# Kernel optimization log

Measured on AMD Instinct MI355X. Metric: run time of the kernel, lower is better.

The kernel has to match this reference:

```python
import jax, jax.numpy as jnp
import numpy as np

B, S, D, H = 4, 2048, 1024, 16
HD = D // H  # head dim = 64


def setup_inputs() -> dict:
    key = jax.random.key(0)
    ks = jax.random.split(key, 11)
    scale = 1.0 / np.sqrt(D)
    return {
        "q": jax.random.normal(ks[0], (B, S, D), jnp.float32),
        "k": jax.random.normal(ks[1], (B, S, D), jnp.float32),
        "v": jax.random.normal(ks[2], (B, S, D), jnp.float32),
        "w_q": jax.random.normal(ks[3], (D, D), jnp.float32) * scale,
        "b_q": jax.random.normal(ks[4], (D,), jnp.float32) * scale,
        "w_k": jax.random.normal(ks[5], (D, D), jnp.float32) * scale,
        "b_k": jax.random.normal(ks[6], (D,), jnp.float32) * scale,
        "w_v": jax.random.normal(ks[7], (D, D), jnp.float32) * scale,
        "b_v": jax.random.normal(ks[8], (D,), jnp.float32) * scale,
        "w_o": jax.random.normal(ks[9], (D, D), jnp.float32) * scale,
        "b_o": jax.random.normal(ks[10], (D,), jnp.float32) * scale,
    }


def _split_heads(x):
    # [B,S,D] -> [B,H,S,HD]
    return x.reshape(B, S, H, HD).transpose(0, 2, 1, 3)


def reference(q, k, v, w_q, b_q, w_k, b_k, w_v, b_v, w_o, b_o):
    qh = _split_heads(q @ w_q + b_q)
    kh = _split_heads(k @ w_k + b_k)
    vh = _split_heads(v @ w_v + b_v)
    # full score matrix [B,H,S,S], as in the naive torch code
    score = jnp.einsum("bhqd,bhkd->bhqk", qh, kh) / jnp.sqrt(jnp.float32(HD))
    attn = jax.nn.softmax(score, axis=-1)
    out = jnp.einsum("bhqk,bhkd->bhqd", attn, vh)
    out = out.transpose(0, 2, 1, 3).reshape(B, S, D)
    return out @ w_o + b_o
```

## Files before the change

### kernel.cpp

```cpp
#include <hip/hip_runtime.h>
#include <hip/hip_bf16.h>

#define BB 4
#define SS 2048
#define DD 1024
#define HH 16
#define HDD 64
#define MM (BB*SS)

using bf16x8 = __attribute__((ext_vector_type(8))) short;
using f32x4  = __attribute__((ext_vector_type(4))) float;
using f32x16 = __attribute__((ext_vector_type(16))) float;

static __device__ __forceinline__ ushort f2bf(float f) {
    __hip_bfloat16 h = __float2bfloat16(f);
    return *reinterpret_cast<ushort*>(&h);
}

static __device__ __forceinline__ void gload_lds16(const ushort* g, ushort* l) {
    __builtin_amdgcn_global_load_lds(
        (const __attribute__((address_space(1))) unsigned int*)g,
        (__attribute__((address_space(3))) unsigned int*)l, 16, 0, 0);
}

static __device__ __forceinline__ unsigned cvtpk(float lo, float hi) {
    unsigned r;
    asm("v_cvt_pk_bf16_f32 %0, %1, %2" : "=v"(r) : "v"(lo), "v"(hi));
    return r;
}

static __device__ __forceinline__ float exp2_raw(float x) {
    float r;
    asm("v_exp_f32 %0, %1" : "=v"(r) : "v"(x));
    return r;
}

static __device__ __forceinline__ void halfswap(unsigned& a, unsigned& b, int hi) {
#if __has_builtin(__builtin_amdgcn_permlane32_swap)
    typedef int v2i __attribute__((ext_vector_type(2)));
    v2i r = __builtin_amdgcn_permlane32_swap((int)a, (int)b, false, false);
    a = (unsigned)r.x; b = (unsigned)r.y;
#else
    unsigned xa = (unsigned)__shfl_xor((int)a, 32);
    unsigned xb = (unsigned)__shfl_xor((int)b, 32);
    unsigned na = hi ? xb : a;
    unsigned nb = hi ? b : xa;
    a = na; b = nb;
#endif
}

#define PIPE_BAR(N) do {                                          \
    asm volatile("s_waitcnt vmcnt(" #N ")" ::: "memory");         \
    __builtin_amdgcn_sched_barrier(0);                            \
    __builtin_amdgcn_s_barrier();                                 \
    __builtin_amdgcn_sched_barrier(0);                            \
} while (0)

__global__ __launch_bounds__(256) void cast3_bf16_k(
    const float* __restrict__ q, const float* __restrict__ k,
    const float* __restrict__ v, ushort* __restrict__ qo,
    ushort* __restrict__ ko, ushort* __restrict__ vo)
{
    const float* in; ushort* out;
    switch (blockIdx.y) {
        case 0:  in = q; out = qo; break;
        case 1:  in = k; out = ko; break;
        default: in = v; out = vo; break;
    }
    const size_t i = ((size_t)blockIdx.x * 256 + threadIdx.x) * 8;
    float4 a = *(const float4*)(in + i);
    float4 b = *(const float4*)(in + i + 4);
    short r[8];
    r[0] = (short)f2bf(a.x); r[1] = (short)f2bf(a.y);
    r[2] = (short)f2bf(a.z); r[3] = (short)f2bf(a.w);
    r[4] = (short)f2bf(b.x); r[5] = (short)f2bf(b.y);
    r[6] = (short)f2bf(b.z); r[7] = (short)f2bf(b.w);
    *(bf16x8*)(out + i) = *(const bf16x8*)r;
}

__global__ __launch_bounds__(256) void wtrans_k(
    const float* __restrict__ w0, const float* __restrict__ w1,
    const float* __restrict__ w2, const float* __restrict__ w3,
    ushort* __restrict__ o0, ushort* __restrict__ o1,
    ushort* __restrict__ o2, ushort* __restrict__ o3)
{
    __shared__ float tile[32][33];
    const float* W; ushort* O;
    switch (blockIdx.z) {
        case 0:  W = w0; O = o0; break;
        case 1:  W = w1; O = o1; break;
        case 2:  W = w2; O = o2; break;
        default: W = w3; O = o3; break;
    }
    const int tx = threadIdx.x & 31, ty = threadIdx.x >> 5;
    const int n0 = blockIdx.x * 32, k0 = blockIdx.y * 32;
    #pragma unroll
    for (int i = 0; i < 4; i++)
        tile[ty * 4 + i][tx] = W[(size_t)(k0 + ty * 4 + i) * DD + n0 + tx];
    __syncthreads();
    #pragma unroll
    for (int i = 0; i < 4; i++)
        O[(size_t)(n0 + ty * 4 + i) * DD + k0 + tx] = f2bf(tile[tx][ty * 4 + i]);
}

template<int MODE>
__global__ __launch_bounds__(256) void gemm_mfma_k(
    const ushort* __restrict__ A, const ushort* __restrict__ WT,
    const float* __restrict__ bias, void* __restrict__ Cout)
{
    __shared__ ushort As[128 * 32];
    __shared__ ushort Bs[128 * 32];

    const int t  = threadIdx.x;
    const int w  = t >> 6;
    const int l  = t & 63;
    const int lr = l & 15;
    const int lg = l >> 4;
    const int wr = w >> 1, wc = w & 1;

    int bid = blockIdx.x;
    bid = (bid & 7) * 64 + (bid >> 3);
    const int mt = bid >> 3, nt = bid & 7;
    const int m0 = mt * 128, n0 = nt * 128;

    const int srow = l >> 2;
    const int scol = (l & 3) * 8;

    f32x4 acc[4][4];
    #pragma unroll
    for (int mi = 0; mi < 4; mi++)
        #pragma unroll
        for (int ni = 0; ni < 4; ni++)
            acc[mi][ni] = (f32x4){0.f, 0.f, 0.f, 0.f};

    const ushort* Ab = A  + (size_t)m0 * DD;
    const ushort* Bb = WT + (size_t)n0 * DD;

    for (int k0 = 0; k0 < DD; k0 += 32) {
        __syncthreads();
        #pragma unroll
        for (int j = 0; j < 2; j++) {
            const int rbase = (w * 2 + j) * 16;
            gload_lds16(Ab + (size_t)(rbase + srow) * DD + k0 + scol, &As[rbase * 32]);
            gload_lds16(Bb + (size_t)(rbase + srow) * DD + k0 + scol, &Bs[rbase * 32]);
        }
        __syncthreads();

        bf16x8 af[4], bfr[4];
        #pragma unroll
        for (int mi = 0; mi < 4; mi++)
            af[mi] = *(const bf16x8*)&As[(wr * 64 + mi * 16 + lr) * 32 + lg * 8];
        #pragma unroll
        for (int ni = 0; ni < 4; ni++)
            bfr[ni] = *(const bf16x8*)&Bs[(wc * 64 + ni * 16 + lr) * 32 + lg * 8];
        #pragma unroll
        for (int mi = 0; mi < 4; mi++)
            #pragma unroll
            for (int ni = 0; ni < 4; ni++)
                acc[mi][ni] = __builtin_amdgcn_mfma_f32_16x16x32_bf16(
                    af[mi], bfr[ni], acc[mi][ni], 0, 0, 0);
    }

    #pragma unroll
    for (int mi = 0; mi < 4; mi++) {
        #pragma unroll
        for (int ni = 0; ni < 4; ni++) {
            const int c  = n0 + wc * 64 + ni * 16 + lr;
            const float bc = bias[c];
            const int r0 = m0 + wr * 64 + mi * 16 + lg * 4;
            if (MODE == 0) {
                float* Co = (float*)Cout;
                #pragma unroll
                for (int rg = 0; rg < 4; rg++)
                    Co[(size_t)(r0 + rg) * DD + c] = acc[mi][ni][rg] + bc;
            } else if (MODE == 3) {
                const int bi = r0 >> 11, si = r0 & 2047;
                const int hi = c >> 6,  hd = c & 63;
                ushort pk[4];
                #pragma unroll
                for (int rg = 0; rg < 4; rg++)
                    pk[rg] = f2bf(acc[mi][ni][rg] + bc);
                ushort* O = (ushort*)Cout;
                *(uint2*)&O[(((size_t)(bi * HH + hi) * HDD) + hd) * SS + si] =
                    *(const uint2*)pk;
            } else {
                const float sc = (MODE == 2) ? 0.180336880111f : 1.0f;
                ushort* O = (ushort*)Cout;
                #pragma unroll
                for (int rg = 0; rg < 4; rg++) {
                    const int r = r0 + rg;
                    const int bi = r >> 11, si = r & 2047;
                    const int hi = c >> 6,  hd = c & 63;
                    O[(((size_t)(bi * HH + hi) * SS) + si) * HDD + hd] =
                        f2bf((acc[mi][ni][rg] + bc) * sc);
                }
            }
        }
    }
}

__global__ __launch_bounds__(256) void flash_attn_mfma(
    const ushort* __restrict__ qh, const ushort* __restrict__ kh,
    const ushort* __restrict__ vt, ushort* __restrict__ ctx)
{
    __shared__ ushort smem[24576];

    const int t  = threadIdx.x;
    const int w  = t >> 6;
    const int l  = t & 63;
    const int hi = l >> 5;
    const int lq = l & 31;

    const int wg = (blockIdx.x & 7) * 128 + (blockIdx.x >> 3);
    const int bi = wg >> 8;
    const int h  = (wg >> 4) & 15;
    const int q0 = (wg & 15) * 128;

    const size_t base  = (size_t)(bi * HH + h) * SS * HDD;
    const size_t basev = (size_t)(bi * HH + h) * HDD * SS;

    bf16x8 qf[4];
    {
        const ushort* qp = qh + base + (size_t)(q0 + w * 32 + lq) * HDD;
        #pragma unroll
        for (int ds = 0; ds < 4; ds++)
            qf[ds] = *(const bf16x8*)(qp + ds * 16 + hi * 8);
    }

    f32x16 o0 = {}, o1 = {};
    float l_loc = 0.f;

    const int rsub = l >> 3;
    const int csw  = ((l & 7) ^ rsub) * 8;
    auto stageK = [&](int buf, int kv) {
        #pragma unroll
        for (int j = 0; j < 2; j++) {
            const int rb = 16 * w + 8 * j;
            gload_lds16(kh + base + (size_t)(kv + rb + rsub) * HDD + csw,
                        &smem[buf * 4096 + rb * 64]);
        }
    };
    auto stageV = [&](int buf, int kv) {
        #pragma unroll
        for (int j = 0; j < 2; j++) {
            const int rb = 16 * w + 8 * j;
            gload_lds16(vt + basev + (size_t)(rb + rsub) * SS + kv + csw,
                        &smem[12288 + buf * 4096 + rb * 64]);
        }
    };

    auto qk = [&](int kbuf, f32x16& s0, f32x16& s1) {
        const ushort* KB = &smem[kbuf * 4096];
        s0 = (f32x16){};
        s1 = (f32x16){};
        __builtin_amdgcn_s_setprio(1);
        #pragma unroll
        for (int ds = 0; ds < 4; ds++) {
            const int slot = ((ds * 2 + hi) ^ (l & 7)) * 8;
            bf16x8 ka0 = *(const bf16x8*)&KB[lq * 64 + slot];
            bf16x8 ka1 = *(const bf16x8*)&KB[(32 + lq) * 64 + slot];
            s0 = __builtin_amdgcn_mfma_f32_32x32x16_bf16(ka0, qf[ds], s0, 0, 0, 0);
            s1 = __builtin_amdgcn_mfma_f32_32x32x16_bf16(ka1, qf[ds], s1, 0, 0, 0);
        }
        __builtin_amdgcn_s_setprio(0);
    };

    auto finish = [&](f32x16& s0, f32x16& s1, bf16x8* pa) {
        float t0 = 0.f, t1 = 0.f, t2 = 0.f, t3 = 0.f;
        #pragma unroll
        for (int r = 0; r < 16; r += 4) {
            s0[r + 0] = exp2_raw(s0[r + 0]); t0 += s0[r + 0];
            s0[r + 1] = exp2_raw(s0[r + 1]); t1 += s0[r + 1];
            s0[r + 2] = exp2_raw(s0[r + 2]); t2 += s0[r + 2];
            s0[r + 3] = exp2_raw(s0[r + 3]); t3 += s0[r + 3];
        }
        #pragma unroll
        for (int r = 0; r < 16; r += 4) {
            s1[r + 0] = exp2_raw(s1[r + 0]); t0 += s1[r + 0];
            s1[r + 1] = exp2_raw(s1[r + 1]); t1 += s1[r + 1];
            s1[r + 2] = exp2_raw(s1[r + 2]); t2 += s1[r + 2];
            s1[r + 3] = exp2_raw(s1[r + 3]); t3 += s1[r + 3];
        }
        l_loc += (t0 + t1) + (t2 + t3);
        #pragma unroll
        for (int sblk = 0; sblk < 4; sblk++) {
            const int ob = (sblk & 1) * 8;
            float e0, e1, e2, e3, e4, e5, e6, e7;
            if (sblk < 2) {
                e0 = s0[ob + 0]; e1 = s0[ob + 1]; e2 = s0[ob + 2]; e3 = s0[ob + 3];
                e4 = s0[ob + 4]; e5 = s0[ob + 5]; e6 = s0[ob + 6]; e7 = s0[ob + 7];
            } else {
                e0 = s1[ob + 0]; e1 = s1[ob + 1]; e2 = s1[ob + 2]; e3 = s1[ob + 3];
                e4 = s1[ob + 4]; e5 = s1[ob + 5]; e6 = s1[ob + 6]; e7 = s1[ob + 7];
            }
            unsigned a = cvtpk(e0, e1);
            unsigned b = cvtpk(e4, e5);
            halfswap(a, b, hi);
            unsigned c = cvtpk(e2, e3);
            unsigned d = cvtpk(e6, e7);
            halfswap(c, d, hi);
            union { unsigned u[4]; bf16x8 v; } fr;
            fr.u[0] = a; fr.u[1] = c; fr.u[2] = b; fr.u[3] = d;
            pa[sblk] = fr.v;
        }
    };

    auto pv = [&](int vbuf, const bf16x8* pa) {
        const ushort* VB = &smem[12288 + vbuf * 4096];
        __builtin_amdgcn_s_setprio(1);
        #pragma unroll
        for (int ks = 0; ks < 4; ks++) {
            const int slot = ((ks * 2 + hi) ^ (l & 7)) * 8;
            bf16x8 vb0 = *(const bf16x8*)&VB[lq * 64 + slot];
            bf16x8 vb1 = *(const bf16x8*)&VB[(32 + lq) * 64 + slot];
            o0 = __builtin_amdgcn_mfma_f32_32x32x16_bf16(pa[ks], vb0, o0, 0, 0, 0);
            o1 = __builtin_amdgcn_mfma_f32_32x32x16_bf16(pa[ks], vb1, o1, 0, 0, 0);
        }
        __builtin_amdgcn_s_setprio(0);
    };

    f32x16 sA0, sA1, sB0, sB1;
    bf16x8 pa[4];
    stageK(0, 0); stageK(1, 64); stageV(0, 0);
    PIPE_BAR(4);
    qk(0, sA0, sA1);

    int ka = 1, kb = 2, kc = 0;
    int va = 0, vb = 1, vc = 2;

    for (int tt = 0; tt < 30; tt += 2) {
        stageK(kb, (tt + 2) * 64);
        PIPE_BAR(2);
        stageV(vb, (tt + 1) * 64);
        qk(ka, sB0, sB1);
        finish(sA0, sA1, pa);
        pv(va, pa);
        { int k2 = ka; ka = kb; kb = kc; kc = k2;
          int v2 = va; va = vb; vb = vc; vc = v2; }

        stageK(kb, (tt + 3) * 64);
        PIPE_BAR(2);
        stageV(vb, (tt + 2) * 64);
        qk(ka, sA0, sA1);
        finish(sB0, sB1, pa);
        pv(va, pa);
        { int k2 = ka; ka = kb; kb = kc; kc = k2;
          int v2 = va; va = vb; vb = vc; vc = v2; }
    }

    PIPE_BAR(0);
    stageV(vb, 31 * 64);
    qk(ka, sB0, sB1);
    finish(sA0, sA1, pa);
    pv(va, pa);
    PIPE_BAR(0);
    finish(sB0, sB1, pa);
    pv(vb, pa);

    const float l_sum = l_loc + __shfl_xor(l_loc, 32);
    const float invl  = 1.0f / l_sum;
    #pragma unroll
    for (int r = 0; r < 16; r++) {
        const int qq = (r & 3) + 8 * (r >> 2) + 4 * hi;
        const float iv = __shfl(invl, qq);
        const int row = q0 + w * 32 + qq;
        ushort* op = ctx + (size_t)(bi * SS + row) * DD + h * HDD;
        op[lq]      = f2bf(o0[r] * iv);
        op[32 + lq] = f2bf(o1[r] * iv);
    }
}

extern "C" void kernel_launch(void* const* d_in, const int* in_sizes, int n_in,
                              void* d_out, int out_size, void* d_ws, size_t ws_size,
                              hipStream_t stream) {
    const float* q   = (const float*)d_in[0];
    const float* k   = (const float*)d_in[1];
    const float* v   = (const float*)d_in[2];
    const float* w_q = (const float*)d_in[3];
    const float* b_q = (const float*)d_in[4];
    const float* w_k = (const float*)d_in[5];
    const float* b_k = (const float*)d_in[6];
    const float* w_v = (const float*)d_in[7];
    const float* b_v = (const float*)d_in[8];
    const float* w_o = (const float*)d_in[9];
    const float* b_o = (const float*)d_in[10];
    float* out = (float*)d_out;

    const size_t SZ = (size_t)BB * SS * DD;
    const size_t WZ = (size_t)DD * DD;
    ushort* ws2  = (ushort*)d_ws;
    ushort* qh   = ws2;
    ushort* kh   = ws2 + SZ;
    ushort* vt   = ws2 + 2 * SZ;
    ushort* ctxb = ws2 + 3 * SZ;
    ushort* qbf  = ws2 + 4 * SZ;
    ushort* kbf  = ws2 + 5 * SZ;
    ushort* vbf  = ws2 + 6 * SZ;
    ushort* wqT  = ws2 + 7 * SZ;
    ushort* wkT  = wqT + WZ;
    ushort* wvT  = wkT + WZ;
    ushort* woT  = wvT + WZ;

    const int castBlocks = (int)(SZ / (256 * 8));
    cast3_bf16_k<<<dim3(castBlocks, 3), 256, 0, stream>>>(q, k, v, qbf, kbf, vbf);
    wtrans_k<<<dim3(32, 32, 4), 256, 0, stream>>>(w_q, w_k, w_v, w_o,
                                                  wqT, wkT, wvT, woT);

    const int gblocks = (MM / 128) * (DD / 128);
    gemm_mfma_k<2><<<gblocks, 256, 0, stream>>>(qbf, wqT, b_q, qh);
    gemm_mfma_k<1><<<gblocks, 256, 0, stream>>>(kbf, wkT, b_k, kh);
    gemm_mfma_k<3><<<gblocks, 256, 0, stream>>>(vbf, wvT, b_v, vt);

    flash_attn_mfma<<<dim3(1024), 256, 0, stream>>>(qh, kh, vt, ctxb);

    gemm_mfma_k<0><<<gblocks, 256, 0, stream>>>(ctxb, woT, b_o, out);
}
```

Baseline: 220.7 us.

## Double query rows per wave in flash attention and simplify to double-buffered pipeline

Each wave now handles 64 query rows (two 32-row groups) instead of 32, so each K/V tile loaded into LDS is reused across twice as many queries and the grid halves to 512 blocks. The triple-buffered K / software-pipelined QK-softmax-PV schedule is replaced with a simpler double-buffered loop that waits on every tile. LDS shrinks and launch bounds request two blocks per CU. This cuts LDS and global traffic per FLOP but raises register pressure and removes overlap of QK with the previous tile's softmax. With 512 blocks on a 256-CU device the occupancy may be thin.

```diff
diff --git a/kernel.cpp b/kernel.cpp
--- a/kernel.cpp
+++ b/kernel.cpp
@@ -199,11 +199,11 @@
     }
 }
 
-__global__ __launch_bounds__(256) void flash_attn_mfma(
+__global__ __launch_bounds__(256, 2) void flash_attn_mfma(
     const ushort* __restrict__ qh, const ushort* __restrict__ kh,
     const ushort* __restrict__ vt, ushort* __restrict__ ctx)
 {
-    __shared__ ushort smem[24576];
+    __shared__ ushort smem[16384];
 
     const int t  = threadIdx.x;
     const int w  = t >> 6;
@@ -211,24 +211,27 @@
     const int hi = l >> 5;
     const int lq = l & 31;
 
-    const int wg = (blockIdx.x & 7) * 128 + (blockIdx.x >> 3);
-    const int bi = wg >> 8;
-    const int h  = (wg >> 4) & 15;
-    const int q0 = (wg & 15) * 128;
+    const int wg = (blockIdx.x & 7) * 64 + (blockIdx.x >> 3);
+    const int bi = wg >> 7;
+    const int h  = (wg >> 3) & 15;
+    const int q0 = (wg & 7) * 256;
 
     const size_t base  = (size_t)(bi * HH + h) * SS * HDD;
     const size_t basev = (size_t)(bi * HH + h) * HDD * SS;
 
-    bf16x8 qf[4];
+    bf16x8 qf0[4], qf1[4];
     {
-        const ushort* qp = qh + base + (size_t)(q0 + w * 32 + lq) * HDD;
-        #pragma unroll
-        for (int ds = 0; ds < 4; ds++)
-            qf[ds] = *(const bf16x8*)(qp + ds * 16 + hi * 8);
-    }
-
-    f32x16 o0 = {}, o1 = {};
-    float l_loc = 0.f;
+        const ushort* qp0 = qh + base + (size_t)(q0 + w * 64 + lq) * HDD;
+        const ushort* qp1 = qp0 + 32 * HDD;
+        #pragma unroll
+        for (int ds = 0; ds < 4; ds++) {
+            qf0[ds] = *(const bf16x8*)(qp0 + ds * 16 + hi * 8);
+            qf1[ds] = *(const bf16x8*)(qp1 + ds * 16 + hi * 8);
+        }
+    }
+
+    f32x16 o00 = {}, o01 = {}, o10 = {}, o11 = {};
+    float l0 = 0.f, l1 = 0.f;
 
     const int rsub = l >> 3;
     const int csw  = ((l & 7) ^ rsub) * 8;
@@ -245,128 +248,108 @@
         for (int j = 0; j < 2; j++) {
             const int rb = 16 * w + 8 * j;
             gload_lds16(vt + basev + (size_t)(rb + rsub) * SS + kv + csw,
-                        &smem[12288 + buf * 4096 + rb * 64]);
+                        &smem[8192 + buf * 4096 + rb * 64]);
         }
     };
 
-    auto qk = [&](int kbuf, f32x16& s0, f32x16& s1) {
-        const ushort* KB = &smem[kbuf * 4096];
-        s0 = (f32x16){};
-        s1 = (f32x16){};
+    auto qk2 = [&](const ushort* KB, int kvh, f32x16& sg0, f32x16& sg1) {
+        sg0 = (f32x16){};
+        sg1 = (f32x16){};
         __builtin_amdgcn_s_setprio(1);
         #pragma unroll
         for (int ds = 0; ds < 4; ds++) {
             const int slot = ((ds * 2 + hi) ^ (l & 7)) * 8;
-            bf16x8 ka0 = *(const bf16x8*)&KB[lq * 64 + slot];
-            bf16x8 ka1 = *(const bf16x8*)&KB[(32 + lq) * 64 + slot];
-            s0 = __builtin_amdgcn_mfma_f32_32x32x16_bf16(ka0, qf[ds], s0, 0, 0, 0);
-            s1 = __builtin_amdgcn_mfma_f32_32x32x16_bf16(ka1, qf[ds], s1, 0, 0, 0);
+            bf16x8 ka = *(const bf16x8*)&KB[(kvh * 32 + lq) * 64 + slot];
+            sg0 = __builtin_amdgcn_mfma_f32_32x32x16_bf16(ka, qf0[ds], sg0, 0, 0, 0);
+            sg1 = __builtin_amdgcn_mfma_f32_32x32x16_bf16(ka, qf1[ds], sg1, 0, 0, 0);
         }
         __builtin_amdgcn_s_setprio(0);
     };
 
-    auto finish = [&](f32x16& s0, f32x16& s1, bf16x8* pa) {
+    auto finish16 = [&](f32x16& s, float& lacc, bf16x8* pa2) {
         float t0 = 0.f, t1 = 0.f, t2 = 0.f, t3 = 0.f;
         #pragma unroll
         for (int r = 0; r < 16; r += 4) {
-            s0[r + 0] = exp2_raw(s0[r + 0]); t0 += s0[r + 0];
-            s0[r + 1] = exp2_raw(s0[r + 1]); t1 += s0[r + 1];
-            s0[r + 2] = exp2_raw(s0[r + 2]); t2 += s0[r + 2];
-            s0[r + 3] = exp2_raw(s0[r + 3]); t3 += s0[r + 3];
-        }
-        #pragma unroll
-        for (int r = 0; r < 16; r += 4) {
-            s1[r + 0] = exp2_raw(s1[r + 0]); t0 += s1[r + 0];
-            s1[r + 1] = exp2_raw(s1[r + 1]); t1 += s1[r + 1];
-            s1[r + 2] = exp2_raw(s1[r + 2]); t2 += s1[r + 2];
-            s1[r + 3] = exp2_raw(s1[r + 3]); t3 += s1[r + 3];
-        }
-        l_loc += (t0 + t1) + (t2 + t3);
-        #pragma unroll
-        for (int sblk = 0; sblk < 4; sblk++) {
-            const int ob = (sblk & 1) * 8;
-            float e0, e1, e2, e3, e4, e5, e6, e7;
-            if (sblk < 2) {
-                e0 = s0[ob + 0]; e1 = s0[ob + 1]; e2 = s0[ob + 2]; e3 = s0[ob + 3];
-                e4 = s0[ob + 4]; e5 = s0[ob + 5]; e6 = s0[ob + 6]; e7 = s0[ob + 7];
-            } else {
-                e0 = s1[ob + 0]; e1 = s1[ob + 1]; e2 = s1[ob + 2]; e3 = s1[ob + 3];
-                e4 = s1[ob + 4]; e5 = s1[ob + 5]; e6 = s1[ob + 6]; e7 = s1[ob + 7];
-            }
-            unsigned a = cvtpk(e0, e1);
-            unsigned b = cvtpk(e4, e5);
+            s[r + 0] = exp2_raw(s[r + 0]); t0 += s[r + 0];
+            s[r + 1] = exp2_raw(s[r + 1]); t1 += s[r + 1];
+            s[r + 2] = exp2_raw(s[r + 2]); t2 += s[r + 2];
+            s[r + 3] = exp2_raw(s[r + 3]); t3 += s[r + 3];
+        }
+        lacc += (t0 + t1) + (t2 + t3);
+        #pragma unroll
+        for (int sblk = 0; sblk < 2; sblk++) {
+            const int ob = sblk * 8;
+            unsigned a = cvtpk(s[ob + 0], s[ob + 1]);
+            unsigned b = cvtpk(s[ob + 4], s[ob + 5]);
             halfswap(a, b, hi);
-            unsigned c = cvtpk(e2, e3);
-            unsigned d = cvtpk(e6, e7);
+            unsigned c = cvtpk(s[ob + 2], s[ob + 3]);
+            unsigned d = cvtpk(s[ob + 6], s[ob + 7]);
             halfswap(c, d, hi);
             union { unsigned u[4]; bf16x8 v; } fr;
             fr.u[0] = a; fr.u[1] = c; fr.u[2] = b; fr.u[3] = d;
-            pa[sblk] = fr.v;
+            pa2[sblk] = fr.v;
         }
     };
 
-    auto pv = [&](int vbuf, const bf16x8* pa) {
-        const ushort* VB = &smem[12288 + vbuf * 4096];
+    auto pvhalf = [&](const ushort* VB, int kvh,
+                      const bf16x8* pg0, const bf16x8* pg1) {
         __builtin_amdgcn_s_setprio(1);
         #pragma unroll
-        for (int ks = 0; ks < 4; ks++) {
+        for (int ksl = 0; ksl < 2; ksl++) {
+            const int ks = kvh * 2 + ksl;
             const int slot = ((ks * 2 + hi) ^ (l & 7)) * 8;
             bf16x8 vb0 = *(const bf16x8*)&VB[lq * 64 + slot];
             bf16x8 vb1 = *(const bf16x8*)&VB[(32 + lq) * 64 + slot];
-            o0 = __builtin_amdgcn_mfma_f32_32x32x16_bf16(pa[ks], vb0, o0, 0, 0, 0);
-            o1 = __builtin_amdgcn_mfma_f32_32x32x16_bf16(pa[ks], vb1, o1, 0, 0, 0);
+            o00 = __builtin_amdgcn_mfma_f32_32x32x16_bf16(pg0[ksl], vb0, o00, 0, 0, 0);
+            o01 = __builtin_amdgcn_mfma_f32_32x32x16_bf16(pg0[ksl], vb1, o01, 0, 0, 0);
+            o10 = __builtin_amdgcn_mfma_f32_32x32x16_bf16(pg1[ksl], vb0, o10, 0, 0, 0);
+            o11 = __builtin_amdgcn_mfma_f32_32x32x16_bf16(pg1[ksl], vb1, o11, 0, 0, 0);
         }
         __builtin_amdgcn_s_setprio(0);
     };
 
-    f32x16 sA0, sA1, sB0, sB1;
-    bf16x8 pa[4];
-    stageK(0, 0); stageK(1, 64); stageV(0, 0);
-    PIPE_BAR(4);
-    qk(0, sA0, sA1);
-
-    int ka = 1, kb = 2, kc = 0;
-    int va = 0, vb = 1, vc = 2;
-
-    for (int tt = 0; tt < 30; tt += 2) {
-        stageK(kb, (tt + 2) * 64);
-        PIPE_BAR(2);
-        stageV(vb, (tt + 1) * 64);
-        qk(ka, sB0, sB1);
-        finish(sA0, sA1, pa);
-        pv(va, pa);
-        { int k2 = ka; ka = kb; kb = kc; kc = k2;
-          int v2 = va; va = vb; vb = vc; vc = v2; }
-
-        stageK(kb, (tt + 3) * 64);
-        PIPE_BAR(2);
-        stageV(vb, (tt + 2) * 64);
-        qk(ka, sA0, sA1);
-        finish(sB0, sB1, pa);
-        pv(va, pa);
-        { int k2 = ka; ka = kb; kb = kc; kc = k2;
-          int v2 = va; va = vb; vb = vc; vc = v2; }
-    }
-
-    PIPE_BAR(0);
-    stageV(vb, 31 * 64);
-    qk(ka, sB0, sB1);
-    finish(sA0, sA1, pa);
-    pv(va, pa);
-    PIPE_BAR(0);
-    finish(sB0, sB1, pa);
-    pv(vb, pa);
-
-    const float l_sum = l_loc + __shfl_xor(l_loc, 32);
-    const float invl  = 1.0f / l_sum;
+    stageK(0, 0); stageV(0, 0);
+    int cur = 0;
+
+    for (int tt = 0; tt < 32; tt++) {
+        PIPE_BAR(0);
+        if (tt + 1 < 32) { stageK(cur ^ 1, (tt + 1) * 64);
+                           stageV(cur ^ 1, (tt + 1) * 64); }
+
+        const ushort* KB = &smem[cur * 4096];
+        const ushort* VB = &smem[8192 + cur * 4096];
+
+        f32x16 sA, sB, sC, sD;
+        qk2(KB, 0, sA, sB);
+        qk2(KB, 1, sC, sD);
+
+        bf16x8 pg0[2], pg1[2];
+        finish16(sA, l0, pg0);
+        finish16(sB, l1, pg1);
+        pvhalf(VB, 0, pg0, pg1);
+        finish16(sC, l0, pg0);
+        finish16(sD, l1, pg1);
+        pvhalf(VB, 1, pg0, pg1);
+
+        cur ^= 1;
+    }
+
+    const float ls0 = l0 + __shfl_xor(l0, 32);
+    const float ls1 = l1 + __shfl_xor(l1, 32);
+    const float iv0 = 1.0f / ls0;
+    const float iv1 = 1.0f / ls1;
     #pragma unroll
     for (int r = 0; r < 16; r++) {
         const int qq = (r & 3) + 8 * (r >> 2) + 4 * hi;
-        const float iv = __shfl(invl, qq);
-        const int row = q0 + w * 32 + qq;
-        ushort* op = ctx + (size_t)(bi * SS + row) * DD + h * HDD;
-        op[lq]      = f2bf(o0[r] * iv);
-        op[32 + lq] = f2bf(o1[r] * iv);
+        const float a0 = __shfl(iv0, qq);
+        const float a1 = __shfl(iv1, qq);
+        const int row0 = q0 + w * 64 + qq;
+        ushort* op0 = ctx + (size_t)(bi * SS + row0) * DD + h * HDD;
+        op0[lq]      = f2bf(o00[r] * a0);
+        op0[32 + lq] = f2bf(o01[r] * a0);
+        ushort* op1 = op0 + (size_t)32 * DD;
+        op1[lq]      = f2bf(o10[r] * a1);
+        op1[32 + lq] = f2bf(o11[r] * a1);
     }
 }
 
@@ -411,7 +394,7 @@
     gemm_mfma_k<1><<<gblocks, 256, 0, stream>>>(kbf, wkT, b_k, kh);
     gemm_mfma_k<3><<<gblocks, 256, 0, stream>>>(vbf, wvT, b_v, vt);
 
-    flash_attn_mfma<<<dim3(1024), 256, 0, stream>>>(qh, kh, vt, ctxb);
+    flash_attn_mfma<<<dim3(512), 256, 0, stream>>>(qh, kh, vt, ctxb);
 
     gemm_mfma_k<0><<<gblocks, 256, 0, stream>>>(ctxb, woT, b_o, out);
 }
```

New measurement: 209.9 us. -4.9%, faster.
